# Kernel optimization log

Hardware: AMD Instinct MI355X
Metric: run time of the kernel (lower is better)

## Reference

```python
import jax, jax.numpy as jnp
import numpy as np
import math

T = 4096      # 2 s @ 2048 Hz (G2Net)
B = 64
NV = 16
SR = 2048.0
FLOW = 20.0
FHIGH = 512.0


def _build_wft():
    """Morlet-like wavelet filter bank in the frequency domain, exactly as in build()."""
    max_scale = T // (np.sqrt(2) * 2)
    if max_scale <= 1:
        max_scale = T // 2
    max_scale = np.floor(NV * np.log2(max_scale))
    scales = 2 * (2 ** (1 / NV)) ** np.arange(0, max_scale + 1)
    frequencies = SR * (6 / (2 * np.pi)) / scales
    frequencies = frequencies[frequencies >= FLOW]
    scales = scales[0:len(frequencies)]
    frequencies = frequencies[frequencies <= FHIGH]
    scales = scales[len(scales) - len(frequencies):len(scales)]
    padvalue = T // 2
    n = padvalue * 2 + T
    omega = np.arange(1, math.floor(n / 2) + 1, dtype=np.float64)
    omega = omega * (2 * np.pi) / n
    omega = np.concatenate((np.array([0.0]), omega,
                            -omega[np.arange(math.floor((n - 1) / 2), 0, -1, dtype=int) - 1]))
    wft = np.zeros([scales.size, omega.size])
    for jj, scale in enumerate(scales):
        expnt = -(scale * omega - 6) ** 2 / 2 * (omega > 0)
        wft[jj, :] = 2 * np.exp(expnt) * (omega > 0)
    return wft.astype(np.float32)  # [num_scales=75, n=8192]


def setup_inputs() -> dict:
    key = jax.random.key(0)
    inputs = jax.random.normal(key, (B, T), dtype=jnp.float32)
    wft = jnp.asarray(_build_wft())
    return {"inputs": inputs, "wft": wft}


def reference(inputs, wft):
    # inputs: [B, T] float32; wft: [S, n] float32 (n = 2*T)
    t = inputs.shape[1]
    pad = t // 2
    # symmetric (endpoint-including) reflect pad, same as tf.reverse of head/tail slices
    x = jnp.concatenate([inputs[:, :pad][:, ::-1], inputs, inputs[:, -pad:][:, ::-1]], axis=1)  # [B, n]
    f = jnp.fft.fft(x.astype(jnp.complex64), axis=-1)                   # [B, n]
    # kron(ones([S,1]), f) * wft  ==  broadcast multiply f[:,None,:] * wft[None]
    cwtcfs = jnp.fft.ifft(f[:, None, :] * wft.astype(jnp.complex64)[None, :, :], axis=-1)  # [B, S, n]
    return jnp.log(jnp.abs(cwtcfs[:, :, pad:pad + t]))                  # [B, S, T]
```

## Files before the change

kernel.cpp:

```cpp
#include <hip/hip_runtime.h>

#define TT 4096
#define NN 8192
#define NF 4096

#define SW(i) ((i) ^ ((((i) >> 4) ^ ((i) >> 8)) & 15))

__device__ __forceinline__ float sin2pi(float x) { return __builtin_amdgcn_sinf(x); }
__device__ __forceinline__ float cos2pi(float x) { return __builtin_amdgcn_cosf(x); }

template<int S>
__device__ __forceinline__ void dft4(float& ar, float& ai, float& br, float& bi,
                                     float& cr, float& ci, float& er, float& ei) {
    float t0r = ar + cr, t0i = ai + ci;
    float t1r = ar - cr, t1i = ai - ci;
    float t2r = br + er, t2i = bi + ei;
    float t3r = br - er, t3i = bi - ei;
    ar = t0r + t2r; ai = t0i + t2i;
    cr = t0r - t2r; ci = t0i - t2i;
    br = t1r - S * t3i; bi = t1i + S * t3r;
    er = t1r + S * t3i; ei = t1i - S * t3r;
}

template<int S>
__device__ __forceinline__ void dft16(float xr[16], float xi[16]) {
    #pragma unroll
    for (int n0 = 0; n0 < 4; ++n0)
        dft4<S>(xr[n0], xi[n0], xr[n0 + 4], xi[n0 + 4],
                xr[n0 + 8], xi[n0 + 8], xr[n0 + 12], xi[n0 + 12]);

    const float C1 = 0.9238795325112867f;
    const float S1 = 0.3826834323650898f;
    const float R2 = 0.7071067811865476f;
    #define TMUL(idx, wr, wi) { float _r = xr[idx]*(wr) - xi[idx]*(wi); \
                                xi[idx] = xr[idx]*(wi) + xi[idx]*(wr); xr[idx] = _r; }
    TMUL(5,  C1,  S * S1)
    TMUL(9,  R2,  S * R2)
    TMUL(13, S1,  S * C1)
    TMUL(6,  R2,  S * R2)
    { float _r = -S * xi[10]; xi[10] = S * xr[10]; xr[10] = _r; }
    TMUL(14, -R2, S * R2)
    TMUL(7,  S1,  S * C1)
    TMUL(11, -R2, S * R2)
    TMUL(15, -C1, -S * S1)
    #undef TMUL

    #pragma unroll
    for (int k0 = 0; k0 < 4; ++k0)
        dft4<S>(xr[4*k0], xi[4*k0], xr[4*k0+1], xi[4*k0+1],
                xr[4*k0+2], xi[4*k0+2], xr[4*k0+3], xi[4*k0+3]);

    float tr[16], ti[16];
    #pragma unroll
    for (int q = 0; q < 16; ++q) { int p = 4*(q & 3) + (q >> 2); tr[q] = xr[p]; ti[q] = xi[p]; }
    #pragma unroll
    for (int q = 0; q < 16; ++q) { xr[q] = tr[q]; xi[q] = ti[q]; }
}

template<int S>
__device__ void fft4096_r16(float2* lds, int tid) {
    float xr[16], xi[16];

    #pragma unroll
    for (int q = 0; q < 16; ++q) {
        float2 v = lds[SW(tid + 256 * q)];
        xr[q] = v.x; xi[q] = v.y;
    }
    dft16<S>(xr, xi);
    #pragma unroll
    for (int q = 1; q < 16; ++q) {
        const float t = (float)(tid * q) * (1.0f / 4096.0f);
        const float wr = cos2pi(t), wi = S * sin2pi(t);
        float r = xr[q] * wr - xi[q] * wi;
        xi[q] = xr[q] * wi + xi[q] * wr;
        xr[q] = r;
    }
    #pragma unroll
    for (int q = 0; q < 16; ++q) lds[SW(tid + 256 * q)] = make_float2(xr[q], xi[q]);
    __syncthreads();

    {
        const int j = tid & 15;
        const int base = ((tid >> 4) << 8) + j;
        #pragma unroll
        for (int q = 0; q < 16; ++q) {
            float2 v = lds[SW(base + 16 * q)];
            xr[q] = v.x; xi[q] = v.y;
        }
        dft16<S>(xr, xi);
        #pragma unroll
        for (int q = 1; q < 16; ++q) {
            const float t = (float)(j * q) * (1.0f / 256.0f);
            const float wr = cos2pi(t), wi = S * sin2pi(t);
            float r = xr[q] * wr - xi[q] * wi;
            xi[q] = xr[q] * wi + xi[q] * wr;
            xr[q] = r;
        }
        #pragma unroll
        for (int q = 0; q < 16; ++q) lds[SW(base + 16 * q)] = make_float2(xr[q], xi[q]);
    }
    __syncthreads();

    {
        const int base = tid << 4;
        const int f2 = (tid ^ (tid >> 4)) & 15;
        #pragma unroll
        for (int q = 0; q < 16; ++q) {
            float2 v = lds[base + (q ^ f2)];
            xr[q] = v.x; xi[q] = v.y;
        }
        dft16<S>(xr, xi);
        __syncthreads();
        const int c = tid & 15;
        const int h = tid >> 4;
        #pragma unroll
        for (int q = 0; q < 16; ++q)
            lds[(q << 8) + (c << 4) + (h ^ c ^ q)] = make_float2(xr[q], xi[q]);
    }
    __syncthreads();
}

template<int S>
__device__ void fft4096_r16x2(float4* lds, int tid) {
    float xr0[16], xi0[16], xr1[16], xi1[16];

    #define CMUL2(q, wr, wi) { \
        float _r0 = xr0[q]*(wr) - xi0[q]*(wi); xi0[q] = xr0[q]*(wi) + xi0[q]*(wr); xr0[q] = _r0; \
        float _r1 = xr1[q]*(wr) - xi1[q]*(wi); xi1[q] = xr1[q]*(wi) + xi1[q]*(wr); xr1[q] = _r1; }

    #pragma unroll
    for (int q = 0; q < 16; ++q) {
        float4 v = lds[SW(tid + 256 * q)];
        xr0[q] = v.x; xi0[q] = v.y; xr1[q] = v.z; xi1[q] = v.w;
    }
    dft16<S>(xr0, xi0);
    dft16<S>(xr1, xi1);
    #pragma unroll
    for (int q = 1; q < 16; ++q) {
        const float t = (float)(tid * q) * (1.0f / 4096.0f);
        const float wr = cos2pi(t), wi = S * sin2pi(t);
        CMUL2(q, wr, wi)
    }
    #pragma unroll
    for (int q = 0; q < 16; ++q)
        lds[SW(tid + 256 * q)] = make_float4(xr0[q], xi0[q], xr1[q], xi1[q]);
    __syncthreads();

    {
        const int j = tid & 15;
        const int base = ((tid >> 4) << 8) + j;
        #pragma unroll
        for (int q = 0; q < 16; ++q) {
            float4 v = lds[SW(base + 16 * q)];
            xr0[q] = v.x; xi0[q] = v.y; xr1[q] = v.z; xi1[q] = v.w;
        }
        dft16<S>(xr0, xi0);
        dft16<S>(xr1, xi1);
        #pragma unroll
        for (int q = 1; q < 16; ++q) {
            const float t = (float)(j * q) * (1.0f / 256.0f);
            const float wr = cos2pi(t), wi = S * sin2pi(t);
            CMUL2(q, wr, wi)
        }
        #pragma unroll
        for (int q = 0; q < 16; ++q)
            lds[SW(base + 16 * q)] = make_float4(xr0[q], xi0[q], xr1[q], xi1[q]);
    }
    __syncthreads();

    {
        const int base = tid << 4;
        const int f2 = (tid ^ (tid >> 4)) & 15;
        #pragma unroll
        for (int q = 0; q < 16; ++q) {
            float4 v = lds[base + (q ^ f2)];
            xr0[q] = v.x; xi0[q] = v.y; xr1[q] = v.z; xi1[q] = v.w;
        }
        dft16<S>(xr0, xi0);
        dft16<S>(xr1, xi1);
        __syncthreads();
        const int c = tid & 15;
        const int h = tid >> 4;
        #pragma unroll
        for (int q = 0; q < 16; ++q)
            lds[(q << 8) + (c << 4) + (h ^ c ^ q)] = make_float4(xr0[q], xi0[q], xr1[q], xi1[q]);
    }
    __syncthreads();
    #undef CMUL2
}

__device__ __forceinline__ int refl(int p) {
    if (p < 2048) return 2047 - p;
    if (p < 6144) return p - 2048;
    return 10239 - p;
}

__global__ __launch_bounds__(256) void fwd_kernel(const float* __restrict__ in,
                                                  float2* __restrict__ F) {
    __shared__ float2 lds[NF];
    const int b = blockIdx.x, tid = threadIdx.x;
    const float* row = in + b * TT;

    for (int i = tid; i < NF; i += 256)
        lds[SW(i)] = make_float2(row[refl(2 * i)], row[refl(2 * i + 1)]);

    fft4096_r16<-1>(lds, tid);

    for (int i = tid; i < NF; i += 256) {
        const int k = i + 1;
        const float2 za = lds[SW(k & (NF - 1))];
        const float2 zb = lds[SW((NF - k) & (NF - 1))];
        const float fer = 0.5f * (za.x + zb.x), fei = 0.5f * (za.y - zb.y);
        const float fo_r = 0.5f * (za.y + zb.y), fo_i = -0.5f * (za.x - zb.x);
        const float t = (float)k * (1.0f / 8192.0f);
        const float c = cos2pi(t), s = sin2pi(t);
        F[b * NF + i] = make_float2(fer + c * fo_r + s * fo_i,
                                    fei + c * fo_i - s * fo_r);
    }
}

__global__ __launch_bounds__(256) void inv_kernel(const float2* __restrict__ F,
                                                  const float* __restrict__ wft,
                                                  float* __restrict__ out,
                                                  int NS) {
    __shared__ float4 lds[NF];
    const int blk = blockIdx.x;
    const int b = blk / NS;
    const int j = blk - b * NS;
    const int tid = threadIdx.x;

    const float2* Frow = F + b * NF;
    const float* wrow = wft + (size_t)j * NN + 1;
    float* orow = out + (size_t)(b * NS + j) * TT;
    const float LOGN = 9.0109131020007136f;
    const float HALF_LN2 = 0.34657359027997264f;

    #pragma unroll
    for (int r = 0; r < 16; ++r) {
        const int k = tid + 256 * r;
        const float2 f = Frow[k];
        const float w = wrow[k];
        const float d0r = f.x * w, d0i = f.y * w;
        const float t = (float)k * (1.0f / 8192.0f);
        const float c = cos2pi(t), s = sin2pi(t);
        const float d1r = d0r * c - d0i * s;
        const float d1i = d0r * s + d0i * c;
        lds[SW(k)] = make_float4(d0r, d0i, d1r, d1i);
    }

    fft4096_r16x2<1>(lds, tid);

    #pragma unroll
    for (int i2 = 0; i2 < 8; ++i2) {
        const int tp = 1024 + tid + 256 * i2;
        const float4 z = lds[SW(tp)];
        const float m0 = z.x * z.x + z.y * z.y;
        const float m1 = z.z * z.z + z.w * z.w;
        const float v0 = HALF_LN2 * __builtin_amdgcn_logf(m0) - LOGN;
        const float v1 = HALF_LN2 * __builtin_amdgcn_logf(m1) - LOGN;
        ((float2*)orow)[tid + 256 * i2] = make_float2(v0, v1);
    }
}

extern "C" void kernel_launch(void* const* d_in, const int* in_sizes, int n_in,
                              void* d_out, int out_size, void* d_ws, size_t ws_size,
                              hipStream_t stream) {
    const float* inputs = (const float*)d_in[0];
    const float* wft = (const float*)d_in[1];
    float* out = (float*)d_out;

    const int B = in_sizes[0] / TT;
    const int NS = in_sizes[1] / NN;

    float2* F = (float2*)d_ws;

    hipLaunchKernelGGL(fwd_kernel, dim3(B), dim3(256), 0, stream, inputs, F);
    hipLaunchKernelGGL(inv_kernel, dim3(B * NS), dim3(256), 0, stream, F, wft, out, NS);
}
```

Measured before the change: 161.2 us.

## Inline FFT stages, use twiddle recurrences, and compute only needed outputs

Inlines the FFT into both kernels so the first radix-16 stage runs straight from registers instead of a round trip through LDS. Per-element sin/cos twiddles are replaced by complex multiplication recurrences, with a reseed at the eighth step to bound error. In the inverse kernel the last radix-16 pass computes and stores only the 8 output bins that fall in the cropped centre window. This cuts transcendental calls, LDS traffic and butterfly work, at the cost of slightly larger rounding error from the recurrences.

```diff
diff --git a/kernel.cpp b/kernel.cpp
--- a/kernel.cpp
+++ b/kernel.cpp
@@ -8,6 +8,12 @@
 
 __device__ __forceinline__ float sin2pi(float x) { return __builtin_amdgcn_sinf(x); }
 __device__ __forceinline__ float cos2pi(float x) { return __builtin_amdgcn_cosf(x); }
+
+#define WMUL(ar, ai, br, bi) { float _t = (ar)*(br) - (ai)*(bi); \
+                               (ai) = (ar)*(bi) + (ai)*(br); (ar) = _t; }
+
+#define C32 0.9807852804032304f
+#define S32 0.19509032201612825f
 
 template<int S>
 __device__ __forceinline__ void dft4(float& ar, float& ai, float& br, float& bi,
@@ -22,6 +28,20 @@
     er = t1r + S * t3i; ei = t1i - S * t3r;
 }
 
+#define DFT16_TMULS(S, xr, xi) { \
+    const float C1 = 0.9238795325112867f; \
+    const float S1 = 0.3826834323650898f; \
+    const float R2 = 0.7071067811865476f; \
+    { float _r = xr[5]*(C1) - xi[5]*(S*S1);  xi[5]  = xr[5]*(S*S1)  + xi[5]*(C1);  xr[5]  = _r; } \
+    { float _r = xr[9]*(R2) - xi[9]*(S*R2);  xi[9]  = xr[9]*(S*R2)  + xi[9]*(R2);  xr[9]  = _r; } \
+    { float _r = xr[13]*(S1) - xi[13]*(S*C1); xi[13] = xr[13]*(S*C1) + xi[13]*(S1); xr[13] = _r; } \
+    { float _r = xr[6]*(R2) - xi[6]*(S*R2);  xi[6]  = xr[6]*(S*R2)  + xi[6]*(R2);  xr[6]  = _r; } \
+    { float _r = -S * xi[10]; xi[10] = S * xr[10]; xr[10] = _r; } \
+    { float _r = xr[14]*(-R2) - xi[14]*(S*R2); xi[14] = xr[14]*(S*R2) + xi[14]*(-R2); xr[14] = _r; } \
+    { float _r = xr[7]*(S1) - xi[7]*(S*C1);  xi[7]  = xr[7]*(S*C1)  + xi[7]*(S1);  xr[7]  = _r; } \
+    { float _r = xr[11]*(-R2) - xi[11]*(S*R2); xi[11] = xr[11]*(S*R2) + xi[11]*(-R2); xr[11] = _r; } \
+    { float _r = xr[15]*(-C1) - xi[15]*(-S*S1); xi[15] = xr[15]*(-S*S1) + xi[15]*(-C1); xr[15] = _r; } }
+
 template<int S>
 __device__ __forceinline__ void dft16(float xr[16], float xi[16]) {
     #pragma unroll
@@ -29,21 +49,7 @@
         dft4<S>(xr[n0], xi[n0], xr[n0 + 4], xi[n0 + 4],
                 xr[n0 + 8], xi[n0 + 8], xr[n0 + 12], xi[n0 + 12]);
 
-    const float C1 = 0.9238795325112867f;
-    const float S1 = 0.3826834323650898f;
-    const float R2 = 0.7071067811865476f;
-    #define TMUL(idx, wr, wi) { float _r = xr[idx]*(wr) - xi[idx]*(wi); \
-                                xi[idx] = xr[idx]*(wi) + xi[idx]*(wr); xr[idx] = _r; }
-    TMUL(5,  C1,  S * S1)
-    TMUL(9,  R2,  S * R2)
-    TMUL(13, S1,  S * C1)
-    TMUL(6,  R2,  S * R2)
-    { float _r = -S * xi[10]; xi[10] = S * xr[10]; xr[10] = _r; }
-    TMUL(14, -R2, S * R2)
-    TMUL(7,  S1,  S * C1)
-    TMUL(11, -R2, S * R2)
-    TMUL(15, -C1, -S * S1)
-    #undef TMUL
+    DFT16_TMULS(S, xr, xi)
 
     #pragma unroll
     for (int k0 = 0; k0 < 4; ++k0)
@@ -58,135 +64,28 @@
 }
 
 template<int S>
-__device__ void fft4096_r16(float2* lds, int tid) {
-    float xr[16], xi[16];
-
-    #pragma unroll
-    for (int q = 0; q < 16; ++q) {
-        float2 v = lds[SW(tid + 256 * q)];
-        xr[q] = v.x; xi[q] = v.y;
-    }
-    dft16<S>(xr, xi);
-    #pragma unroll
-    for (int q = 1; q < 16; ++q) {
-        const float t = (float)(tid * q) * (1.0f / 4096.0f);
-        const float wr = cos2pi(t), wi = S * sin2pi(t);
-        float r = xr[q] * wr - xi[q] * wi;
-        xi[q] = xr[q] * wi + xi[q] * wr;
-        xr[q] = r;
-    }
-    #pragma unroll
-    for (int q = 0; q < 16; ++q) lds[SW(tid + 256 * q)] = make_float2(xr[q], xi[q]);
-    __syncthreads();
-
-    {
-        const int j = tid & 15;
-        const int base = ((tid >> 4) << 8) + j;
-        #pragma unroll
-        for (int q = 0; q < 16; ++q) {
-            float2 v = lds[SW(base + 16 * q)];
-            xr[q] = v.x; xi[q] = v.y;
-        }
-        dft16<S>(xr, xi);
-        #pragma unroll
-        for (int q = 1; q < 16; ++q) {
-            const float t = (float)(j * q) * (1.0f / 256.0f);
-            const float wr = cos2pi(t), wi = S * sin2pi(t);
-            float r = xr[q] * wr - xi[q] * wi;
-            xi[q] = xr[q] * wi + xi[q] * wr;
-            xr[q] = r;
-        }
-        #pragma unroll
-        for (int q = 0; q < 16; ++q) lds[SW(base + 16 * q)] = make_float2(xr[q], xi[q]);
-    }
-    __syncthreads();
-
-    {
-        const int base = tid << 4;
-        const int f2 = (tid ^ (tid >> 4)) & 15;
-        #pragma unroll
-        for (int q = 0; q < 16; ++q) {
-            float2 v = lds[base + (q ^ f2)];
-            xr[q] = v.x; xi[q] = v.y;
-        }
-        dft16<S>(xr, xi);
-        __syncthreads();
-        const int c = tid & 15;
-        const int h = tid >> 4;
-        #pragma unroll
-        for (int q = 0; q < 16; ++q)
-            lds[(q << 8) + (c << 4) + (h ^ c ^ q)] = make_float2(xr[q], xi[q]);
-    }
-    __syncthreads();
-}
-
-template<int S>
-__device__ void fft4096_r16x2(float4* lds, int tid) {
-    float xr0[16], xi0[16], xr1[16], xi1[16];
-
-    #define CMUL2(q, wr, wi) { \
-        float _r0 = xr0[q]*(wr) - xi0[q]*(wi); xi0[q] = xr0[q]*(wi) + xi0[q]*(wr); xr0[q] = _r0; \
-        float _r1 = xr1[q]*(wr) - xi1[q]*(wi); xi1[q] = xr1[q]*(wi) + xi1[q]*(wr); xr1[q] = _r1; }
-
-    #pragma unroll
-    for (int q = 0; q < 16; ++q) {
-        float4 v = lds[SW(tid + 256 * q)];
-        xr0[q] = v.x; xi0[q] = v.y; xr1[q] = v.z; xi1[q] = v.w;
-    }
-    dft16<S>(xr0, xi0);
-    dft16<S>(xr1, xi1);
-    #pragma unroll
-    for (int q = 1; q < 16; ++q) {
-        const float t = (float)(tid * q) * (1.0f / 4096.0f);
-        const float wr = cos2pi(t), wi = S * sin2pi(t);
-        CMUL2(q, wr, wi)
-    }
-    #pragma unroll
-    for (int q = 0; q < 16; ++q)
-        lds[SW(tid + 256 * q)] = make_float4(xr0[q], xi0[q], xr1[q], xi1[q]);
-    __syncthreads();
-
-    {
-        const int j = tid & 15;
-        const int base = ((tid >> 4) << 8) + j;
-        #pragma unroll
-        for (int q = 0; q < 16; ++q) {
-            float4 v = lds[SW(base + 16 * q)];
-            xr0[q] = v.x; xi0[q] = v.y; xr1[q] = v.z; xi1[q] = v.w;
-        }
-        dft16<S>(xr0, xi0);
-        dft16<S>(xr1, xi1);
-        #pragma unroll
-        for (int q = 1; q < 16; ++q) {
-            const float t = (float)(j * q) * (1.0f / 256.0f);
-            const float wr = cos2pi(t), wi = S * sin2pi(t);
-            CMUL2(q, wr, wi)
-        }
-        #pragma unroll
-        for (int q = 0; q < 16; ++q)
-            lds[SW(base + 16 * q)] = make_float4(xr0[q], xi0[q], xr1[q], xi1[q]);
-    }
-    __syncthreads();
-
-    {
-        const int base = tid << 4;
-        const int f2 = (tid ^ (tid >> 4)) & 15;
-        #pragma unroll
-        for (int q = 0; q < 16; ++q) {
-            float4 v = lds[base + (q ^ f2)];
-            xr0[q] = v.x; xi0[q] = v.y; xr1[q] = v.z; xi1[q] = v.w;
-        }
-        dft16<S>(xr0, xi0);
-        dft16<S>(xr1, xi1);
-        __syncthreads();
-        const int c = tid & 15;
-        const int h = tid >> 4;
-        #pragma unroll
-        for (int q = 0; q < 16; ++q)
-            lds[(q << 8) + (c << 4) + (h ^ c ^ q)] = make_float4(xr0[q], xi0[q], xr1[q], xi1[q]);
-    }
-    __syncthreads();
-    #undef CMUL2
+__device__ __forceinline__ void dft16_mid8(float xr[16], float xi[16],
+                                           float yr[8], float yi[8]) {
+    #pragma unroll
+    for (int n0 = 0; n0 < 4; ++n0)
+        dft4<S>(xr[n0], xi[n0], xr[n0 + 4], xi[n0 + 4],
+                xr[n0 + 8], xi[n0 + 8], xr[n0 + 12], xi[n0 + 12]);
+
+    DFT16_TMULS(S, xr, xi)
+
+    #pragma unroll
+    for (int k0 = 0; k0 < 4; ++k0) {
+        float ar = xr[4*k0],     ai = xi[4*k0];
+        float br = xr[4*k0 + 1], bi = xi[4*k0 + 1];
+        float cr = xr[4*k0 + 2], ci = xi[4*k0 + 2];
+        float er = xr[4*k0 + 3], ei = xi[4*k0 + 3];
+        float t0r = ar + cr, t0i = ai + ci;
+        float t1r = ar - cr, t1i = ai - ci;
+        float t2r = br + er, t2i = bi + ei;
+        float t3r = br - er, t3i = bi - ei;
+        yr[k0]     = t1r - S * t3i;  yi[k0]     = t1i + S * t3r;
+        yr[4 + k0] = t0r - t2r;      yi[4 + k0] = t0i - t2i;
+    }
 }
 
 __device__ __forceinline__ int refl(int p) {
@@ -201,21 +100,94 @@
     const int b = blockIdx.x, tid = threadIdx.x;
     const float* row = in + b * TT;
 
-    for (int i = tid; i < NF; i += 256)
-        lds[SW(i)] = make_float2(row[refl(2 * i)], row[refl(2 * i + 1)]);
-
-    fft4096_r16<-1>(lds, tid);
-
-    for (int i = tid; i < NF; i += 256) {
-        const int k = i + 1;
-        const float2 za = lds[SW(k & (NF - 1))];
-        const float2 zb = lds[SW((NF - k) & (NF - 1))];
-        const float fer = 0.5f * (za.x + zb.x), fei = 0.5f * (za.y - zb.y);
-        const float fo_r = 0.5f * (za.y + zb.y), fo_i = -0.5f * (za.x - zb.x);
-        const float t = (float)k * (1.0f / 8192.0f);
-        const float c = cos2pi(t), s = sin2pi(t);
-        F[b * NF + i] = make_float2(fer + c * fo_r + s * fo_i,
-                                    fei + c * fo_i - s * fo_r);
+    float xr[16], xi[16];
+
+    #pragma unroll
+    for (int r = 0; r < 16; ++r) {
+        const int i = tid + 256 * r;
+        xr[r] = row[refl(2 * i)];
+        xi[r] = row[refl(2 * i + 1)];
+    }
+    dft16<-1>(xr, xi);
+    {
+        const float w1r = cos2pi((float)tid * (1.0f / 4096.0f));
+        const float w1i = -sin2pi((float)tid * (1.0f / 4096.0f));
+        const float w8r = cos2pi((float)tid * (1.0f / 512.0f));
+        const float w8i = -sin2pi((float)tid * (1.0f / 512.0f));
+        float wr = w1r, wi = w1i;
+        #pragma unroll
+        for (int q = 1; q < 16; ++q) {
+            float _r = xr[q]*wr - xi[q]*wi;
+            xi[q] = xr[q]*wi + xi[q]*wr; xr[q] = _r;
+            if (q == 7) { wr = w8r; wi = w8i; }
+            else        { WMUL(wr, wi, w1r, w1i) }
+        }
+    }
+    #pragma unroll
+    for (int q = 0; q < 16; ++q) lds[SW(tid + 256 * q)] = make_float2(xr[q], xi[q]);
+    __syncthreads();
+
+    {
+        const int j = tid & 15;
+        const int base = ((tid >> 4) << 8) + j;
+        #pragma unroll
+        for (int q = 0; q < 16; ++q) {
+            float2 v = lds[SW(base + 16 * q)];
+            xr[q] = v.x; xi[q] = v.y;
+        }
+        dft16<-1>(xr, xi);
+        const float w1r = cos2pi((float)j * (1.0f / 256.0f));
+        const float w1i = -sin2pi((float)j * (1.0f / 256.0f));
+        const float w8r = cos2pi((float)j * (1.0f / 32.0f));
+        const float w8i = -sin2pi((float)j * (1.0f / 32.0f));
+        float wr = w1r, wi = w1i;
+        #pragma unroll
+        for (int q = 1; q < 16; ++q) {
+            float _r = xr[q]*wr - xi[q]*wi;
+            xi[q] = xr[q]*wi + xi[q]*wr; xr[q] = _r;
+            if (q == 7) { wr = w8r; wi = w8i; }
+            else        { WMUL(wr, wi, w1r, w1i) }
+        }
+        #pragma unroll
+        for (int q = 0; q < 16; ++q) lds[SW(base + 16 * q)] = make_float2(xr[q], xi[q]);
+    }
+    __syncthreads();
+
+    {
+        const int base = tid << 4;
+        const int f2 = (tid ^ (tid >> 4)) & 15;
+        #pragma unroll
+        for (int q = 0; q < 16; ++q) {
+            float2 v = lds[base + (q ^ f2)];
+            xr[q] = v.x; xi[q] = v.y;
+        }
+        dft16<-1>(xr, xi);
+        __syncthreads();
+        const int c = tid & 15;
+        const int h = tid >> 4;
+        #pragma unroll
+        for (int q = 0; q < 16; ++q)
+            lds[(q << 8) + (c << 4) + (h ^ c ^ q)] = make_float2(xr[q], xi[q]);
+    }
+    __syncthreads();
+
+    {
+        const float c0 = cos2pi((float)(tid + 1) * (1.0f / 8192.0f));
+        const float s0 = sin2pi((float)(tid + 1) * (1.0f / 8192.0f));
+        float cc = c0, ss = s0;
+        #pragma unroll
+        for (int r = 0; r < 16; ++r) {
+            const int i = tid + 256 * r;
+            const int k = i + 1;
+            const float2 za = lds[SW(k & (NF - 1))];
+            const float2 zb = lds[SW((NF - k) & (NF - 1))];
+            const float fer = 0.5f * (za.x + zb.x), fei = 0.5f * (za.y - zb.y);
+            const float fo_r = 0.5f * (za.y + zb.y), fo_i = -0.5f * (za.x - zb.x);
+            F[b * NF + i] = make_float2(fer + cc * fo_r + ss * fo_i,
+                                        fei + cc * fo_i - ss * fo_r);
+            if (r == 7) { cc = -s0; ss = c0; }
+            else        { WMUL(cc, ss, C32, S32) }
+        }
     }
 }
 
@@ -235,20 +207,101 @@
     const float LOGN = 9.0109131020007136f;
     const float HALF_LN2 = 0.34657359027997264f;
 
-    #pragma unroll
-    for (int r = 0; r < 16; ++r) {
-        const int k = tid + 256 * r;
-        const float2 f = Frow[k];
-        const float w = wrow[k];
-        const float d0r = f.x * w, d0i = f.y * w;
-        const float t = (float)k * (1.0f / 8192.0f);
-        const float c = cos2pi(t), s = sin2pi(t);
-        const float d1r = d0r * c - d0i * s;
-        const float d1i = d0r * s + d0i * c;
-        lds[SW(k)] = make_float4(d0r, d0i, d1r, d1i);
-    }
-
-    fft4096_r16x2<1>(lds, tid);
+    float xr0[16], xi0[16], xr1[16], xi1[16];
+
+    #define CMUL2(q, wr, wi) { \
+        float _r0 = xr0[q]*(wr) - xi0[q]*(wi); xi0[q] = xr0[q]*(wi) + xi0[q]*(wr); xr0[q] = _r0; \
+        float _r1 = xr1[q]*(wr) - xi1[q]*(wi); xi1[q] = xr1[q]*(wi) + xi1[q]*(wr); xr1[q] = _r1; }
+
+    {
+        const float c0 = cos2pi((float)tid * (1.0f / 8192.0f));
+        const float s0 = sin2pi((float)tid * (1.0f / 8192.0f));
+        float cr = c0, ci = s0;
+        #pragma unroll
+        for (int r = 0; r < 16; ++r) {
+            const int k = tid + 256 * r;
+            const float2 f = Frow[k];
+            const float w = wrow[k];
+            const float d0r = f.x * w, d0i = f.y * w;
+            xr0[r] = d0r; xi0[r] = d0i;
+            xr1[r] = d0r * cr - d0i * ci;
+            xi1[r] = d0r * ci + d0i * cr;
+            if (r == 7) { cr = -s0; ci = c0; }
+            else        { WMUL(cr, ci, C32, S32) }
+        }
+    }
+    dft16<1>(xr0, xi0);
+    dft16<1>(xr1, xi1);
+    {
+        const float w1r = cos2pi((float)tid * (1.0f / 4096.0f));
+        const float w1i = sin2pi((float)tid * (1.0f / 4096.0f));
+        const float w8r = cos2pi((float)tid * (1.0f / 512.0f));
+        const float w8i = sin2pi((float)tid * (1.0f / 512.0f));
+        float wr = w1r, wi = w1i;
+        #pragma unroll
+        for (int q = 1; q < 16; ++q) {
+            CMUL2(q, wr, wi)
+            if (q == 7) { wr = w8r; wi = w8i; }
+            else        { WMUL(wr, wi, w1r, w1i) }
+        }
+    }
+    #pragma unroll
+    for (int q = 0; q < 16; ++q)
+        lds[SW(tid + 256 * q)] = make_float4(xr0[q], xi0[q], xr1[q], xi1[q]);
+    __syncthreads();
+
+    {
+        const int jj = tid & 15;
+        const int base = ((tid >> 4) << 8) + jj;
+        #pragma unroll
+        for (int q = 0; q < 16; ++q) {
+            float4 v = lds[SW(base + 16 * q)];
+            xr0[q] = v.x; xi0[q] = v.y; xr1[q] = v.z; xi1[q] = v.w;
+        }
+        dft16<1>(xr0, xi0);
+        dft16<1>(xr1, xi1);
+        const float w1r = cos2pi((float)jj * (1.0f / 256.0f));
+        const float w1i = sin2pi((float)jj * (1.0f / 256.0f));
+        const float w8r = cos2pi((float)jj * (1.0f / 32.0f));
+        const float w8i = sin2pi((float)jj * (1.0f / 32.0f));
+        float wr = w1r, wi = w1i;
+        #pragma unroll
+        for (int q = 1; q < 16; ++q) {
+            CMUL2(q, wr, wi)
+            if (q == 7) { wr = w8r; wi = w8i; }
+            else        { WMUL(wr, wi, w1r, w1i) }
+        }
+        #pragma unroll
+        for (int q = 0; q < 16; ++q)
+            lds[SW(base + 16 * q)] = make_float4(xr0[q], xi0[q], xr1[q], xi1[q]);
+    }
+    __syncthreads();
+
+    {
+        const int base = tid << 4;
+        const int f2 = (tid ^ (tid >> 4)) & 15;
+        #pragma unroll
+        for (int q = 0; q < 16; ++q) {
+            float4 v = lds[base + (q ^ f2)];
+            xr0[q] = v.x; xi0[q] = v.y; xr1[q] = v.z; xi1[q] = v.w;
+        }
+        float yr0[8], yi0[8], yr1[8], yi1[8];
+        dft16_mid8<1>(xr0, xi0, yr0, yi0);
+        dft16_mid8<1>(xr1, xi1, yr1, yi1);
+        __syncthreads();
+        const int c = tid & 15;
+        const int h = tid >> 4;
+        #pragma unroll
+        for (int k0 = 0; k0 < 4; ++k0) {
+            const int qa = 4 + k0;
+            const int qb = 8 + k0;
+            lds[(qa << 8) + (c << 4) + (h ^ c ^ qa)] =
+                make_float4(yr0[k0], yi0[k0], yr1[k0], yi1[k0]);
+            lds[(qb << 8) + (c << 4) + (h ^ c ^ qb)] =
+                make_float4(yr0[4 + k0], yi0[4 + k0], yr1[4 + k0], yi1[4 + k0]);
+        }
+    }
+    __syncthreads();
 
     #pragma unroll
     for (int i2 = 0; i2 < 8; ++i2) {
@@ -260,6 +313,7 @@
         const float v1 = HALF_LN2 * __builtin_amdgcn_logf(m1) - LOGN;
         ((float2*)orow)[tid + 256 * i2] = make_float2(v0, v1);
     }
+    #undef CMUL2
 }
 
 extern "C" void kernel_launch(void* const* d_in, const int* in_sizes, int n_in,
```

Measured after the change: 151.3 us. 1.07x faster.
